# Optimization experiments

Hardware: AMD Instinct MI355X
Metric: run time of the kernel (lower is better)

The kernel has to match this reference:

```python
import jax, jax.numpy as jnp
import numpy as np

EMBED_DIM = 1024
NUM_HEADS = 16
HEAD_DIM = EMBED_DIM // NUM_HEADS
NUM_FEATS = 256
YAT_EPS = 0.1
BATCH = 4
SEQ = 4096


def setup_inputs() -> dict:
    key = jax.random.key(0)
    ks = jax.random.split(key, 6)
    s = 1.0 / np.sqrt(EMBED_DIM)
    return {
        "x": jax.random.normal(ks[0], (BATCH, SEQ, EMBED_DIM), jnp.float32),
        "Wq": jax.random.normal(ks[1], (EMBED_DIM, EMBED_DIM), jnp.float32) * s,
        "bq": jnp.zeros((EMBED_DIM,), jnp.float32),
        "Wk": jax.random.normal(ks[2], (EMBED_DIM, EMBED_DIM), jnp.float32) * s,
        "bk": jnp.zeros((EMBED_DIM,), jnp.float32),
        "Wv": jax.random.normal(ks[3], (EMBED_DIM, EMBED_DIM), jnp.float32) * s,
        "bv": jnp.zeros((EMBED_DIM,), jnp.float32),
        "Wo": jax.random.normal(ks[4], (EMBED_DIM, EMBED_DIM), jnp.float32) * s,
        "bo": jnp.zeros((EMBED_DIM,), jnp.float32),
        "projection": jax.random.normal(ks[5], (NUM_HEADS, NUM_FEATS, HEAD_DIM), jnp.float32),
    }


def _spherical_features(x, projection):
    # x: (b, h, s, d) -> (b, h, s, f)
    x_norm = x / (jnp.linalg.norm(x, axis=-1, keepdims=True) + 1e-8)
    proj = jnp.einsum('bhsd,hfd->bhsf', x_norm, projection)
    return jax.nn.relu(proj) + YAT_EPS


def reference(x, Wq, bq, Wk, bk, Wv, bv, Wo, bo, projection):
    b, s, _ = x.shape
    def heads(t):
        return jnp.transpose(t.reshape(b, s, NUM_HEADS, HEAD_DIM), (0, 2, 1, 3))
    Q = heads(x @ Wq + bq)
    K = heads(x @ Wk + bk)
    V = heads(x @ Wv + bv)
    Qp = _spherical_features(Q, projection)  # (b,h,s,f)
    Kp = _spherical_features(K, projection)
    KV = jnp.einsum('bhsf,bhsd->bhfd', Kp, V)           # (b,h,f,d)
    QKV = jnp.einsum('bhsf,bhfd->bhsd', Qp, KV)          # (b,h,s,d)
    K_sum = jnp.sum(Kp, axis=2)                          # (b,h,f)
    normalizer = jnp.einsum('bhsf,bhf->bhs', Qp, K_sum)[..., None]
    normalizer = jnp.maximum(normalizer, 1e-6)
    out = QKV / normalizer
    out = jnp.transpose(out, (0, 2, 1, 3)).reshape(b, s, EMBED_DIM)
    return out @ Wo + bo
```

## Files before the change

### kernel.cpp

```cpp
#include <hip/hip_runtime.h>
#include <stdint.h>

typedef __bf16 bf16_t;
typedef __bf16 bf16x4 __attribute__((ext_vector_type(4)));
typedef __bf16 bf16x8 __attribute__((ext_vector_type(8)));
typedef float  f32x4  __attribute__((ext_vector_type(4)));
typedef unsigned short u16x8 __attribute__((ext_vector_type(8)));
typedef unsigned int u32;

typedef __attribute__((address_space(1))) const uint32_t gas_u32;
typedef __attribute__((address_space(3))) uint32_t las_u32;

#define MFMA16(a, b, c) __builtin_amdgcn_mfma_f32_16x16x32_bf16((a), (b), (c), 0, 0, 0)
#define SBAR() __builtin_amdgcn_s_barrier()
#define WAIT_LGKM0() asm volatile("s_waitcnt lgkmcnt(0)")

__device__ __forceinline__ void gl_lds16(const bf16_t* g, bf16_t* l) {
    __builtin_amdgcn_global_load_lds((gas_u32*)g, (las_u32*)l, 16, 0, 0);
}

__global__ __launch_bounds__(256) void castbf(const float* __restrict__ X,
                                              bf16_t* __restrict__ Xb)
{
    size_t i = ((size_t)blockIdx.x * 256 + threadIdx.x) * 8;
    float4 a = *(const float4*)&X[i];
    float4 b = *(const float4*)&X[i + 4];
    bf16x8 o;
    o[0] = (bf16_t)a.x; o[1] = (bf16_t)a.y; o[2] = (bf16_t)a.z; o[3] = (bf16_t)a.w;
    o[4] = (bf16_t)b.x; o[5] = (bf16_t)b.y; o[6] = (bf16_t)b.z; o[7] = (bf16_t)b.w;
    *(bf16x8*)&Xb[i] = o;
}

__global__ __launch_bounds__(256) void ktrans(
    const float* __restrict__ W0, const float* __restrict__ W1,
    const float* __restrict__ W2, const float* __restrict__ W3,
    bf16_t* __restrict__ WT)
{
    __shared__ float t[64 * 68];
    const int z = blockIdx.z;
    const float* W = (z == 0) ? W0 : (z == 1) ? W1 : (z == 2) ? W2 : W3;
    bf16_t* O = WT + (size_t)z * 1024 * 1024;
    const int r0 = blockIdx.y * 64, c0 = blockIdx.x * 64;
    const int tid = threadIdx.x;
    const int row = tid >> 2, colg = (tid & 3) * 16;
#pragma unroll
    for (int p = 0; p < 4; ++p)
        *(float4*)&t[row * 68 + colg + p * 4] =
            *(const float4*)&W[(size_t)(r0 + row) * 1024 + c0 + colg + p * 4];
    __syncthreads();
    bf16x8 v0, v1;
#pragma unroll
    for (int j = 0; j < 8; ++j) {
        v0[j] = (bf16_t)t[(colg + j) * 68 + row];
        v1[j] = (bf16_t)t[(colg + 8 + j) * 68 + row];
    }
    *(bf16x8*)&O[(size_t)(c0 + row) * 1024 + r0 + colg] = v0;
    *(bf16x8*)&O[(size_t)(c0 + row) * 1024 + r0 + colg + 8] = v1;
}

template <int CMODE, typename OutT>
__global__ __launch_bounds__(512, 2) void gemm256(
    const bf16_t* __restrict__ A, const bf16_t* __restrict__ Bt,
    const float* __restrict__ b0, const float* __restrict__ b1,
    const float* __restrict__ b2, OutT* __restrict__ C,
    int M, int N, int K)
{
    __shared__ bf16_t lds[2][2][256 * 64];
    const int tid = threadIdx.x;
    const int lane = tid & 63, wave = tid >> 6;
    const int q = lane >> 4, ln = lane & 15;
    const int m0 = blockIdx.x * 256, n0 = blockIdx.y * 256;
    const int wm = (wave >> 2) * 128, wn = (wave & 3) * 64;
    const int NT = K >> 6;

    const bf16_t* Ag = A + (size_t)m0 * K;
    const bf16_t* Bg = Bt + (size_t)n0 * K;

    const bf16_t* gstage[4][2];
    bf16_t* lstage[4][2];
#pragma unroll
    for (int cs = 0; cs < 4; ++cs) {
        const int mat = cs >> 1, half = cs & 1;
#pragma unroll
        for (int r = 0; r < 2; ++r) {
            int idx = r * 512 + tid;
            int ri = idx >> 3;
            int row = mat ? (half * 32 + (ri & 31) + ((ri & ~31) << 1))
                          : (half * 64 + (ri & 63) + ((ri & 64) << 1));
            int gs = (idx & 7) ^ (row & 7);
            gstage[cs][r] = (mat ? Bg : Ag) + (size_t)row * K + gs * 8;
            lstage[cs][r] = &lds[0][mat][row * 64 + (idx & 7) * 8];
        }
    }
    auto stage = [&](int cs, int tt) {
        const int koff = tt << 6;
        const int bsel = (tt & 1) << 15;
#pragma unroll
        for (int r = 0; r < 2; ++r)
            gl_lds16(gstage[cs][r] + koff, lstage[cs][r] + bsel);
    };

    int aoff[2][4][2], boff[2][2][2];
#pragma unroll
    for (int mh = 0; mh < 2; ++mh)
#pragma unroll
        for (int mf = 0; mf < 4; ++mf)
#pragma unroll
            for (int ks = 0; ks < 2; ++ks) {
                int row = wm + (mh * 4 + mf) * 16 + ln;
                int g = ((ks << 2) + q) ^ (row & 7);
                aoff[mh][mf][ks] = row * 64 + g * 8;
            }
#pragma unroll
    for (int nh = 0; nh < 2; ++nh)
#pragma unroll
        for (int nf = 0; nf < 2; ++nf)
#pragma unroll
            for (int ks = 0; ks < 2; ++ks) {
                int row = wn + (nh * 2 + nf) * 16 + ln;
                int g = ((ks << 2) + q) ^ (row & 7);
                boff[nh][nf][ks] = row * 64 + g * 8;
            }
    bf16_t* ldsA = &lds[0][0][0];
    bf16_t* ldsB = &lds[0][1][0];

    bf16x8 aL[4][2], bL0[2][2], bL1[2][2];
    auto lda = [&](int mh, int cur) {
        const int b = cur << 15;
#pragma unroll
        for (int mf = 0; mf < 4; ++mf)
#pragma unroll
            for (int ks = 0; ks < 2; ++ks)
                aL[mf][ks] = *(const bf16x8*)&ldsA[b + aoff[mh][mf][ks]];
    };
    auto ldb = [&](bf16x8 (&bL)[2][2], int nh, int cur) {
        const int b = cur << 15;
#pragma unroll
        for (int nf = 0; nf < 2; ++nf)
#pragma unroll
            for (int ks = 0; ks < 2; ++ks)
                bL[nf][ks] = *(const bf16x8*)&ldsB[b + boff[nh][nf][ks]];
    };

    f32x4 acc[8][4] = {};
    auto mm = [&](bf16x8 (&bL)[2][2], int mh, int nh) {
        __builtin_amdgcn_s_setprio(1);
#pragma unroll
        for (int mf = 0; mf < 4; ++mf)
#pragma unroll
            for (int nf = 0; nf < 2; ++nf)
#pragma unroll
                for (int ks = 0; ks < 2; ++ks)
                    acc[mh * 4 + mf][nh * 2 + nf] =
                        MFMA16(aL[mf][ks], bL[nf][ks], acc[mh * 4 + mf][nh * 2 + nf]);
        __builtin_amdgcn_s_setprio(0);
    };

    stage(0, 0); stage(2, 0); stage(3, 0); stage(1, 0);
    stage(0, 1); stage(2, 1); stage(3, 1);
    asm volatile("s_waitcnt vmcnt(6)");
    __builtin_amdgcn_sched_barrier(0);
    SBAR();

    for (int t = 0; t < NT; ++t) {
        const int cur = t & 1;
        lda(0, cur); ldb(bL0, 0, cur);
        if (t + 1 < NT) stage(1, t + 1);
        SBAR(); WAIT_LGKM0();
        mm(bL0, 0, 0);
        SBAR();
        ldb(bL1, 1, cur);
        if (t + 2 < NT) stage(0, t + 2);
        SBAR(); WAIT_LGKM0();
        mm(bL1, 0, 1);
        SBAR();
        lda(1, cur);
        if (t + 2 < NT) stage(2, t + 2);
        SBAR(); WAIT_LGKM0();
        mm(bL0, 1, 0);
        SBAR();
        if (t + 2 < NT) stage(3, t + 2);
        SBAR();
        mm(bL1, 1, 1);
        if (t + 2 < NT) asm volatile("s_waitcnt vmcnt(6)");
        else            asm volatile("s_waitcnt vmcnt(0)");
        __builtin_amdgcn_sched_barrier(0);
        SBAR();
    }
    __syncthreads();

    if (CMODE == 0) {
        float* myCf = (float*)&lds[0][0][0] + wave * 1088;
        const int nf0 = n0 + wn;
        const int mfst = m0 + wm;
#pragma unroll
        for (int mt = 0; mt < 8; ++mt) {
#pragma unroll
            for (int nt = 0; nt < 4; ++nt) {
                float bv = b0[nf0 + nt * 16 + ln];
#pragma unroll
                for (int r = 0; r < 4; ++r)
                    myCf[(q * 4 + r) * 68 + nt * 16 + ln] = acc[mt][nt][r] + bv;
            }
#pragma unroll
            for (int c = 0; c < 4; ++c) {
                int flat = c * 64 + lane;
                int rr = flat >> 4, co = (flat & 15) * 4;
                f32x4 v = *(const f32x4*)&myCf[rr * 68 + co];
                *(f32x4*)&C[(size_t)(mfst + mt * 16 + rr) * N + nf0 + co] = v;
            }
        }
    } else {
        bf16_t* myCs = &lds[0][0][0] + wave * 2304;
        const int n_first = n0 + wn;
        const int t_ = n_first >> 10;
        const int h = (n_first >> 6) & 15;
        const float* bp = (t_ == 0) ? b0 : (t_ == 1) ? b1 : b2;
        const int m_first = m0 + wm;
        const int bI = m_first >> 12, s0 = m_first & 4095;
        bf16_t* Cp = (bf16_t*)C + (size_t)t_ * 16777216 + (size_t)(bI * 16 + h) * 262144;
#pragma unroll
        for (int p = 0; p < 4; ++p) {
#pragma unroll
            for (int mh2 = 0; mh2 < 2; ++mh2) {
                int mf = p * 2 + mh2;
#pragma unroll
                for (int nt = 0; nt < 4; ++nt) {
                    float bv = bp[(n_first + nt * 16 + ln) & 1023];
#pragma unroll
                    for (int r = 0; r < 4; ++r)
                        myCs[(mh2 * 16 + q * 4 + r) * 72 + nt * 16 + ln] =
                            (bf16_t)(acc[mf][nt][r] + bv);
                }
            }
#pragma unroll
            for (int c = 0; c < 4; ++c) {
                int flat = c * 64 + lane;
                int rr = flat >> 3, co = (flat & 7) * 8;
                bf16x8 v = *(const bf16x8*)&myCs[rr * 72 + co];
                *(bf16x8*)&Cp[(size_t)(s0 + p * 32 + rr) * 64 + co] = v;
            }
            __syncthreads();
        }
    }
}

__global__ __launch_bounds__(256) void kside(
    const bf16_t* __restrict__ Khm, const bf16_t* __restrict__ Vhm,
    const bf16_t* __restrict__ proj, float* __restrict__ P)
{
    __shared__ bf16_t Kn[64 * 72];
    __shared__ bf16_t KpT[256 * 72];
    __shared__ bf16_t Vt[80 * 72];
    const int tid = threadIdx.x;
    const int lane = tid & 63, wave = tid >> 6;
    const int q = lane >> 4, ln = lane & 15;
    const int bh = blockIdx.x, c = blockIdx.y;

    const bf16_t* Kh = Khm + (size_t)bh * 262144;
    const bf16_t* Vh = Vhm + (size_t)bh * 262144;
    const bf16_t* pr = proj + (size_t)(bh & 15) * 16384;

    for (int i = tid; i < 16 * 72; i += 256) {
        int rr = i / 72, cc = i % 72;
        Vt[(64 + rr) * 72 + cc] = (rr == 0) ? (bf16_t)1.0f : (bf16_t)0.0f;
    }
    bf16x8 pf[4][2];
#pragma unroll
    for (int nt = 0; nt < 4; ++nt)
#pragma unroll
        for (int ks = 0; ks < 2; ++ks)
            pf[nt][ks] = *(const bf16x8*)&pr[(size_t)(wave * 64 + nt * 16 + ln) * 64 + ks * 32 + q * 8];

    f32x4 kv[4][5] = {};
    const int s_base = c * 512;
    const int s2 = tid >> 3, vD = (tid & 7) * 8;
    for (int st = 0; st < 8; ++st) {
        const int s0 = s_base + st * 64;
        {
            const bf16_t* rp = &Kh[(size_t)(s0 + wave * 16 + ln) * 64 + q * 8];
            bf16x8 a0 = *(const bf16x8*)rp;
            bf16x8 a1 = *(const bf16x8*)(rp + 32);
            float f[16], ss = 0.f;
#pragma unroll
            for (int i = 0; i < 8; ++i) { f[i] = (float)a0[i]; f[8 + i] = (float)a1[i]; }
#pragma unroll
            for (int i = 0; i < 16; ++i) ss += f[i] * f[i];
            ss += __shfl_xor(ss, 16, 64);
            ss += __shfl_xor(ss, 32, 64);
            float sc = 1.0f / (sqrtf(ss) + 1e-8f);
            bf16x8 na0, na1;
#pragma unroll
            for (int i = 0; i < 8; ++i) {
                na0[i] = (bf16_t)(f[i] * sc);
                na1[i] = (bf16_t)(f[8 + i] * sc);
            }
            *(bf16x8*)&Kn[(wave * 16 + ln) * 72 + q * 8] = na0;
            *(bf16x8*)&Kn[(wave * 16 + ln) * 72 + 32 + q * 8] = na1;
        }
        __syncthreads();
        f32x4 fa[4][4] = {};
#pragma unroll
        for (int mt = 0; mt < 4; ++mt) {
            bf16x8 n0v = *(const bf16x8*)&Kn[(mt * 16 + ln) * 72 + q * 8];
            bf16x8 n1v = *(const bf16x8*)&Kn[(mt * 16 + ln) * 72 + 32 + q * 8];
#pragma unroll
            for (int nt = 0; nt < 4; ++nt) {
                fa[mt][nt] = MFMA16(n0v, pf[nt][0], fa[mt][nt]);
                fa[mt][nt] = MFMA16(n1v, pf[nt][1], fa[mt][nt]);
            }
        }
        __syncthreads();
#pragma unroll
        for (int mt = 0; mt < 4; ++mt)
#pragma unroll
            for (int nt = 0; nt < 4; ++nt) {
                bf16x4 kp;
#pragma unroll
                for (int r = 0; r < 4; ++r)
                    kp[r] = (bf16_t)(fmaxf(fa[mt][nt][r], 0.0f) + 0.1f);
                *(bf16x4*)&KpT[(wave * 64 + nt * 16 + ln) * 72 + mt * 16 + q * 4] = kp;
            }
        {
            u16x8 v0 = *(const u16x8*)&Vh[(size_t)(s0 + 2 * s2) * 64 + vD];
            u16x8 v1 = *(const u16x8*)&Vh[(size_t)(s0 + 2 * s2 + 1) * 64 + vD];
#pragma unroll
            for (int e = 0; e < 8; ++e) {
                u32 w = (u32)v0[e] | ((u32)v1[e] << 16);
                *(u32*)&Vt[(vD + e) * 72 + 2 * s2] = w;
            }
        }
        __syncthreads();
#pragma unroll
        for (int ks = 0; ks < 2; ++ks)
#pragma unroll
            for (int mt = 0; mt < 4; ++mt) {
                bf16x8 a = *(const bf16x8*)&KpT[(wave * 64 + mt * 16 + ln) * 72 + ks * 32 + q * 8];
#pragma unroll
                for (int nt = 0; nt < 5; ++nt) {
                    bf16x8 bb = *(const bf16x8*)&Vt[(nt * 16 + ln) * 72 + ks * 32 + q * 8];
                    kv[mt][nt] = MFMA16(a, bb, kv[mt][nt]);
                }
            }
    }
    float* Pp = P + (size_t)(bh * 8 + c) * 65 * 256;
#pragma unroll
    for (int mt = 0; mt < 4; ++mt)
#pragma unroll
        for (int nt = 0; nt < 5; ++nt)
            if (nt < 4 || ln == 0)
                *(f32x4*)&Pp[(size_t)(nt * 16 + ln) * 256 + wave * 64 + mt * 16 + q * 4] = kv[mt][nt];
}

__global__ __launch_bounds__(256) void kreduce(const float* __restrict__ P, bf16_t* __restrict__ KVt)
{
    size_t i = (size_t)blockIdx.x * 256 + threadIdx.x;
    int f = (int)(i & 255);
    int n = (int)((i >> 8) % 80);
    int bh = (int)(i / (256 * 80));
    float s = 0.f;
    if (n < 65) {
        const float* p = P + (size_t)bh * 8 * 65 * 256 + (size_t)n * 256 + f;
#pragma unroll
        for (int c = 0; c < 8; ++c) s += p[(size_t)c * 65 * 256];
    }
    KVt[i] = (bf16_t)s;
}

__global__ __launch_bounds__(256) void qside(
    const bf16_t* __restrict__ Qhm, const bf16_t* __restrict__ proj,
    const bf16_t* __restrict__ KVt, bf16_t* __restrict__ attn)
{
    __shared__ bf16_t Qp[128 * 136];
    const int tid = threadIdx.x;
    const int lane = tid & 63, wave = tid >> 6;
    const int q = lane >> 4, ln = lane & 15;
    const int bh = blockIdx.x, stile = blockIdx.y;
    const int bI = bh >> 4, h = bh & 15;

    const bf16_t* Qh = Qhm + (size_t)bh * 262144 + (size_t)stile * 128 * 64;
    const bf16_t* pr = proj + (size_t)h * 16384;
    const bf16_t* kv = KVt + (size_t)bh * 20480;

    bf16x8 na[2][2];
#pragma unroll
    for (int mt = 0; mt < 2; ++mt) {
        const bf16_t* rp = &Qh[(size_t)(wave * 32 + mt * 16 + ln) * 64 + q * 8];
        bf16x8 a0 = *(const bf16x8*)rp;
        bf16x8 a1 = *(const bf16x8*)(rp + 32);
        float f[16], ss = 0.f;
#pragma unroll
        for (int i = 0; i < 8; ++i) { f[i] = (float)a0[i]; f[8 + i] = (float)a1[i]; }
#pragma unroll
        for (int i = 0; i < 16; ++i) ss += f[i] * f[i];
        ss += __shfl_xor(ss, 16, 64);
        ss += __shfl_xor(ss, 32, 64);
        float sc = 1.0f / (sqrtf(ss) + 1e-8f);
#pragma unroll
        for (int i = 0; i < 8; ++i) {
            na[mt][0][i] = (bf16_t)(f[i] * sc);
            na[mt][1][i] = (bf16_t)(f[8 + i] * sc);
        }
    }

    f32x4 oacc[2][5] = {};
#pragma unroll
    for (int fh = 0; fh < 2; ++fh) {
        f32x4 fa[2][8] = {};
#pragma unroll
        for (int ks = 0; ks < 2; ++ks) {
            bf16x8 bb[8];
#pragma unroll
            for (int nt = 0; nt < 8; ++nt)
                bb[nt] = *(const bf16x8*)&pr[(size_t)(fh * 128 + nt * 16 + ln) * 64 + ks * 32 + q * 8];
#pragma unroll
            for (int mt = 0; mt < 2; ++mt)
#pragma unroll
                for (int nt = 0; nt < 8; ++nt)
                    fa[mt][nt] = MFMA16(na[mt][ks], bb[nt], fa[mt][nt]);
        }
#pragma unroll
        for (int mt = 0; mt < 2; ++mt)
#pragma unroll
            for (int nt = 0; nt < 8; ++nt)
#pragma unroll
                for (int r = 0; r < 4; ++r)
                    Qp[(wave * 32 + mt * 16 + q * 4 + r) * 136 + nt * 16 + ln] =
                        (bf16_t)(fmaxf(fa[mt][nt][r], 0.0f) + 0.1f);
#pragma unroll
        for (int ks = 0; ks < 4; ++ks) {
            bf16x8 aa[2];
#pragma unroll
            for (int mt = 0; mt < 2; ++mt)
                aa[mt] = *(const bf16x8*)&Qp[(wave * 32 + mt * 16 + ln) * 136 + ks * 32 + q * 8];
#pragma unroll
            for (int nt = 0; nt < 5; ++nt) {
                bf16x8 bb = *(const bf16x8*)&kv[(size_t)(nt * 16 + ln) * 256 + fh * 128 + ks * 32 + q * 8];
#pragma unroll
                for (int mt = 0; mt < 2; ++mt)
                    oacc[mt][nt] = MFMA16(aa[mt], bb, oacc[mt][nt]);
            }
        }
    }
    bf16_t* Ap = attn + ((size_t)(bI * 4096 + stile * 128) * 1024) + h * 64;
#pragma unroll
    for (int mt = 0; mt < 2; ++mt)
#pragma unroll
        for (int r = 0; r < 4; ++r) {
            float nrm = fmaxf(__shfl(oacc[mt][4][r], lane & 48, 64), 1e-6f);
            int sl = wave * 32 + mt * 16 + q * 4 + r;
#pragma unroll
            for (int nt = 0; nt < 4; ++nt)
                Ap[(size_t)sl * 1024 + nt * 16 + ln] = (bf16_t)(oacc[mt][nt][r] / nrm);
        }
}

extern "C" void kernel_launch(void* const* d_in, const int* in_sizes, int n_in,
                              void* d_out, int out_size, void* d_ws, size_t ws_size,
                              hipStream_t stream)
{
    const float* x = (const float*)d_in[0];
    const float* Wq = (const float*)d_in[1];
    const float* bq = (const float*)d_in[2];
    const float* Wk = (const float*)d_in[3];
    const float* bk = (const float*)d_in[4];
    const float* Wv = (const float*)d_in[5];
    const float* bv = (const float*)d_in[6];
    const float* Wo = (const float*)d_in[7];
    const float* bo = (const float*)d_in[8];
    const float* proj = (const float*)d_in[9];

    char* ws = (char*)d_ws;
    bf16_t* WT = (bf16_t*)(ws);
    bf16_t* projb = (bf16_t*)(ws + (8ull << 20));
    bf16_t* KVt = (bf16_t*)(ws + (9ull << 20));
    bf16_t* Q = (bf16_t*)(ws + (12ull << 20));
    bf16_t* K = (bf16_t*)(ws + (44ull << 20));
    bf16_t* V = (bf16_t*)(ws + (76ull << 20));
    bf16_t* xb = (bf16_t*)(ws + (108ull << 20));
    float* P = (float*)xb;
    bf16_t* attn = V;
    float* out = (float*)d_out;

    castbf<<<8192, 256, 0, stream>>>(x, xb);
    castbf<<<128, 256, 0, stream>>>(proj, projb);
    ktrans<<<dim3(16, 16, 4), 256, 0, stream>>>(Wq, Wk, Wv, Wo, WT);
    gemm256<2, bf16_t><<<dim3(64, 12), 512, 0, stream>>>(
        xb, WT, bq, bk, bv, Q, 16384, 3072, 1024);
    kside<<<dim3(64, 8), 256, 0, stream>>>(K, V, projb, P);
    kreduce<<<5120, 256, 0, stream>>>(P, KVt);
    qside<<<dim3(64, 32), 256, 0, stream>>>(Q, projb, KVt, attn);
    gemm256<0, float><<<dim3(64, 4), 512, 0, stream>>>(
        attn, WT + 3ull * 1048576, bo, bo, bo, out, 16384, 1024, 1024);
}
```

Baseline: 399.5 us.

## Compute transposed feature tiles in qside and pass them via lane shuffles instead of LDS

In the qside kernel the MFMA operands are swapped so the feature and output tiles come out transposed. The relu+eps features are packed to bf16 pairs in registers and moved into the second matmul's B-operand layout with cross-lane shuffles, removing the 34 KB shared-memory staging buffer and its store/load round trip. The output store becomes a 4-wide bf16 vector per lane. The cost is many more shuffle (ds_bpermute) instructions and higher register pressure, while LDS use drops, which may allow more blocks per CU.

```diff
diff --git a/kernel.cpp b/kernel.cpp
--- a/kernel.cpp
+++ b/kernel.cpp
@@ -371,7 +371,6 @@
     const bf16_t* __restrict__ Qhm, const bf16_t* __restrict__ proj,
     const bf16_t* __restrict__ KVt, bf16_t* __restrict__ attn)
 {
-    __shared__ bf16_t Qp[128 * 136];
     const int tid = threadIdx.x;
     const int lane = tid & 63, wave = tid >> 6;
     const int q = lane >> 4, ln = lane & 15;
@@ -403,56 +402,81 @@
         }
     }
 
-    f32x4 oacc[2][5] = {};
+    f32x4 oaccT[5][2] = {};
+    const int sl0 = (q & 1) * 32 + ln;
 #pragma unroll
     for (int fh = 0; fh < 2; ++fh) {
-        f32x4 fa[2][8] = {};
+        f32x4 fat[8][2] = {};
 #pragma unroll
         for (int ks = 0; ks < 2; ++ks) {
-            bf16x8 bb[8];
+            bf16x8 pa[8];
 #pragma unroll
             for (int nt = 0; nt < 8; ++nt)
-                bb[nt] = *(const bf16x8*)&pr[(size_t)(fh * 128 + nt * 16 + ln) * 64 + ks * 32 + q * 8];
-#pragma unroll
-            for (int mt = 0; mt < 2; ++mt)
-#pragma unroll
-                for (int nt = 0; nt < 8; ++nt)
-                    fa[mt][nt] = MFMA16(na[mt][ks], bb[nt], fa[mt][nt]);
-        }
-#pragma unroll
-        for (int mt = 0; mt < 2; ++mt)
+                pa[nt] = *(const bf16x8*)&pr[(size_t)(fh * 128 + nt * 16 + ln) * 64 + ks * 32 + q * 8];
 #pragma unroll
             for (int nt = 0; nt < 8; ++nt)
 #pragma unroll
-                for (int r = 0; r < 4; ++r)
-                    Qp[(wave * 32 + mt * 16 + q * 4 + r) * 136 + nt * 16 + ln] =
-                        (bf16_t)(fmaxf(fa[mt][nt][r], 0.0f) + 0.1f);
+                for (int mt = 0; mt < 2; ++mt)
+                    fat[nt][mt] = MFMA16(pa[nt], na[mt][ks], fat[nt][mt]);
+        }
+        u32 w0[8][2], w1[8][2];
+#pragma unroll
+        for (int nt = 0; nt < 8; ++nt)
+#pragma unroll
+            for (int mt = 0; mt < 2; ++mt) {
+                union { bf16_t h[2]; u32 u; } p0, p1;
+                p0.h[0] = (bf16_t)(fmaxf(fat[nt][mt][0], 0.0f) + 0.1f);
+                p0.h[1] = (bf16_t)(fmaxf(fat[nt][mt][1], 0.0f) + 0.1f);
+                p1.h[0] = (bf16_t)(fmaxf(fat[nt][mt][2], 0.0f) + 0.1f);
+                p1.h[1] = (bf16_t)(fmaxf(fat[nt][mt][3], 0.0f) + 0.1f);
+                w0[nt][mt] = p0.u;
+                w1[nt][mt] = p1.u;
+            }
 #pragma unroll
         for (int ks = 0; ks < 4; ++ks) {
-            bf16x8 aa[2];
-#pragma unroll
-            for (int mt = 0; mt < 2; ++mt)
-                aa[mt] = *(const bf16x8*)&Qp[(wave * 32 + mt * 16 + ln) * 136 + ks * 32 + q * 8];
+            bf16x8 Bf[2];
+#pragma unroll
+            for (int mt = 0; mt < 2; ++mt) {
+                u32 t00 = __shfl(w0[2 * ks][mt],     sl0, 64);
+                u32 t01 = __shfl(w1[2 * ks][mt],     sl0, 64);
+                u32 t10 = __shfl(w0[2 * ks + 1][mt], sl0, 64);
+                u32 t11 = __shfl(w1[2 * ks + 1][mt], sl0, 64);
+                u32 u00 = __shfl(w0[2 * ks][mt],     sl0 + 16, 64);
+                u32 u01 = __shfl(w1[2 * ks][mt],     sl0 + 16, 64);
+                u32 u10 = __shfl(w0[2 * ks + 1][mt], sl0 + 16, 64);
+                u32 u11 = __shfl(w1[2 * ks + 1][mt], sl0 + 16, 64);
+                const bool hi = (q >= 2);
+                union { u32 u[4]; bf16x8 v; } pk;
+                pk.u[0] = hi ? t10 : t00;
+                pk.u[1] = hi ? t11 : t01;
+                pk.u[2] = hi ? u10 : u00;
+                pk.u[3] = hi ? u11 : u01;
+                Bf[mt] = pk.v;
+            }
 #pragma unroll
             for (int nt = 0; nt < 5; ++nt) {
-                bf16x8 bb = *(const bf16x8*)&kv[(size_t)(nt * 16 + ln) * 256 + fh * 128 + ks * 32 + q * 8];
+                bf16x8 Af = *(const bf16x8*)&kv[(size_t)(nt * 16 + ln) * 256 + fh * 128 + ks * 32 + q * 8];
 #pragma unroll
                 for (int mt = 0; mt < 2; ++mt)
-                    oacc[mt][nt] = MFMA16(aa[mt], bb, oacc[mt][nt]);
+                    oaccT[nt][mt] = MFMA16(Af, Bf[mt], oaccT[nt][mt]);
             }
         }
     }
     bf16_t* Ap = attn + ((size_t)(bI * 4096 + stile * 128) * 1024) + h * 64;
 #pragma unroll
-    for (int mt = 0; mt < 2; ++mt)
-#pragma unroll
-        for (int r = 0; r < 4; ++r) {
-            float nrm = fmaxf(__shfl(oacc[mt][4][r], lane & 48, 64), 1e-6f);
-            int sl = wave * 32 + mt * 16 + q * 4 + r;
-#pragma unroll
-            for (int nt = 0; nt < 4; ++nt)
-                Ap[(size_t)sl * 1024 + nt * 16 + ln] = (bf16_t)(oacc[mt][nt][r] / nrm);
-        }
+    for (int mt = 0; mt < 2; ++mt) {
+        float nv = __shfl(oaccT[4][mt][0], ln, 64);
+        float nrm = fmaxf(nv, 1e-6f);
+        const int srow = wave * 32 + mt * 16 + ln;
+#pragma unroll
+        for (int nt = 0; nt < 4; ++nt) {
+            bf16x4 o;
+#pragma unroll
+            for (int r = 0; r < 4; ++r)
+                o[r] = (bf16_t)(oaccT[nt][mt][r] / nrm);
+            *(bf16x4*)&Ap[(size_t)srow * 1024 + nt * 16 + q * 4] = o;
+        }
+    }
 }
 
 extern "C" void kernel_launch(void* const* d_in, const int* in_sizes, int n_in,
```

New measurement: 399.6 us. No clear change (+0.0%).
